# Optimization experiments

Hardware: AMD Instinct MI355X
Metric: run time of the kernel (lower is better)

Reference implementation:

```python
import jax, jax.numpy as jnp
import numpy as np

K = 3; PAD = 1; STRIDE = 1; EPS = 1e-5


def setup_inputs() -> dict:
    key = jax.random.key(0)
    k0, k1, k2 = jax.random.split(key, 3)
    B, C, H, W, O = 4, 256, 64, 64, 256
    x = jax.random.normal(k0, (B, C, H, W), jnp.float32)
    # offset conv: small random weights so offsets are nontrivial but bounded
    w_off = jax.random.normal(k1, (2 * K * K, C, K, K), jnp.float32) * 0.01
    b_off = jnp.zeros((2 * K * K,), jnp.float32)
    # kaiming normal, mode=fan_out: std = sqrt(2 / (O*K*K))
    w_def = jax.random.normal(k2, (O, C, K, K), jnp.float32) * np.float32(np.sqrt(2.0 / (O * K * K)))
    gamma = jnp.ones((O,), jnp.float32)
    beta = jnp.zeros((O,), jnp.float32)
    return {"x": x, "w_off": w_off, "b_off": b_off, "w_def": w_def, "gamma": gamma, "beta": beta}


def _bilinear_gather(x, py, px):
    """x: [B,C,H,W]; py,px: [B,K2,Ho,Wo] float sample coords.
    Returns [B,K2,Ho,Wo,C] with zero padding outside (per-corner masking,
    matching torchvision deform_conv2d)."""
    B, C, H, W = x.shape
    y0f = jnp.floor(py); x0f = jnp.floor(px)
    wy1 = py - y0f; wy0 = 1.0 - wy1
    wx1 = px - x0f; wx0 = 1.0 - wx1
    bidx = jnp.arange(B)[:, None, None, None]

    def corner(yf, xf, wgt):
        valid = (yf >= 0) & (yf <= H - 1) & (xf >= 0) & (xf <= W - 1)
        yc = jnp.clip(yf.astype(jnp.int32), 0, H - 1)
        xc = jnp.clip(xf.astype(jnp.int32), 0, W - 1)
        v = x[bidx, :, yc, xc]  # [B,K2,Ho,Wo,C] (advanced idx moves C last)
        return v * (wgt * valid)[..., None]

    return (corner(y0f, x0f, wy0 * wx0) + corner(y0f, x0f + 1.0, wy0 * wx1)
            + corner(y0f + 1.0, x0f, wy1 * wx0) + corner(y0f + 1.0, x0f + 1.0, wy1 * wx1))


def _forward(x, w_off, b_off, w_def, gamma, beta):
    B, C, H, W = x.shape
    O = w_def.shape[0]
    K2 = K * K
    # 1) offset-predicting conv
    off = jax.lax.conv_general_dilated(x, w_off, (STRIDE, STRIDE), ((PAD, PAD), (PAD, PAD)))
    off = off + b_off[None, :, None, None]
    Ho, Wo = off.shape[2], off.shape[3]
    off = off.reshape(B, K2, 2, Ho, Wo)  # pairs (dy, dx) per kernel tap
    # 2) deformable sampling locations
    ky, kx = jnp.meshgrid(jnp.arange(K, dtype=jnp.float32), jnp.arange(K, dtype=jnp.float32), indexing='ij')
    base_y = (jnp.arange(Ho, dtype=jnp.float32) * STRIDE - PAD)
    base_x = (jnp.arange(Wo, dtype=jnp.float32) * STRIDE - PAD)
    py = off[:, :, 0] + ky.reshape(K2)[None, :, None, None] + base_y[None, None, :, None]
    px = off[:, :, 1] + kx.reshape(K2)[None, :, None, None] + base_x[None, None, None, :]
    vals = _bilinear_gather(x, py, px)  # [B,K2,Ho,Wo,C]
    # 3) deform conv GEMM (bias=False)
    out = jnp.einsum('bkhwc,ock->bohw', vals, w_def.reshape(O, C, K2))
    # 4) BatchNorm (training mode: batch stats) + ReLU
    mean = out.mean(axis=(0, 2, 3))
    var = out.var(axis=(0, 2, 3))
    out = (out - mean[None, :, None, None]) * (gamma * jax.lax.rsqrt(var + EPS))[None, :, None, None]
    out = out + beta[None, :, None, None]
    return jax.nn.relu(out)


def reference(x, w_off, b_off, w_def, gamma, beta):
    return _forward(x, w_off, b_off, w_def, gamma, beta)
```

## Files before the change

kernel.cpp:

```cpp
#include <hip/hip_runtime.h>
#include <hip/hip_bf16.h>

typedef unsigned int  uint;
typedef unsigned short ushort;
typedef short bf16x8 __attribute__((ext_vector_type(8)));
typedef float f32x4  __attribute__((ext_vector_type(4)));

#define HW   4096
#define KD   2304

__device__ __forceinline__ void load_lds16(const void* g, void* l) {
    __builtin_amdgcn_global_load_lds((const __attribute__((address_space(1))) void*)g,
                                     (__attribute__((address_space(3))) void*)l, 16, 0, 0);
}
__device__ __forceinline__ float blo(uint u) { return __uint_as_float(u << 16); }
__device__ __forceinline__ float bhi(uint u) { return __uint_as_float(u & 0xffff0000u); }
__device__ __forceinline__ uint pack2(float e, float o) {
    __hip_bfloat16 he = __float2bfloat16(e), ho = __float2bfloat16(o);
    return (uint)(*(ushort*)&he) | ((uint)(*(ushort*)&ho) << 16);
}

__global__ __launch_bounds__(256) void prep_all(const float* __restrict__ x,
                                                const float* __restrict__ w_def,
                                                const float* __restrict__ w_off,
                                                uint* __restrict__ x2t,
                                                ushort* __restrict__ bt,
                                                ushort* __restrict__ bt0,
                                                float* __restrict__ stats) {
    __shared__ uint tl[32][65];
    int bid = blockIdx.x;
    int t = threadIdx.x;
    if (bid < 1024) {
        int ab  = bid & 63;
        int cpb = (bid >> 6) & 3;
        int b   = bid >> 8;
#pragma unroll
        for (int i = 0; i < 8; ++i) {
            int idx = i * 256 + t;
            int cp = idx >> 6, a = idx & 63;
            const float* p = x + ((size_t)(b * 256 + (cpb * 32 + cp) * 2)) * HW + ab * 64 + a;
            tl[cp][a] = pack2(p[0], p[HW]);
        }
        __syncthreads();
#pragma unroll
        for (int i = 0; i < 8; ++i) {
            int idx = i * 256 + t;
            int a = idx >> 5, cp = idx & 31;
            x2t[((size_t)b * 4096 + ab * 64 + a) * 128 + cpb * 32 + cp] = tl[cp][a];
        }
    } else if (bid < 3328) {
        int idx = (bid - 1024) * 256 + t;
        int c   = idx & 255;
        int tap = (idx >> 8) % 9;
        int o   = idx / KD;
        __hip_bfloat16 h = __float2bfloat16(w_def[(o * 256 + c) * 9 + tap]);
        bt[idx] = *(ushort*)&h;
    } else if (bid < 3616) {
        int idx = (bid - 3328) * 256 + t;
        int c   = idx & 255;
        int tap = (idx >> 8) % 9;
        int j   = idx / KD;
        float v = (j < 18) ? w_off[(j * 256 + c) * 9 + tap] : 0.f;
        __hip_bfloat16 h = __float2bfloat16(v);
        bt0[idx] = *(ushort*)&h;
    } else {
        float4 z = {0.f, 0.f, 0.f, 0.f};
        ((float4*)stats)[t] = z;
    }
}

__global__ __attribute__((amdgpu_waves_per_eu(4, 4))) __launch_bounds__(1024)
void fused_main(const uint* __restrict__ x2t,
                const ushort* __restrict__ bt,
                const ushort* __restrict__ bt0,
                const float* __restrict__ b_off,
                float* __restrict__ out,
                float* __restrict__ stats) {
    int id = blockIdx.x;
    int xcd = id & 7;
    int b = xcd >> 1, h = (xcd & 1) * 32 + (id >> 3);
    int t = threadIdx.x;
    int wv = t >> 6, lane = t & 63;
    int mrow = lane & 15, quad = lane >> 4;
    bool producer = (wv < 8);
    int ppos = (wv << 3) + (lane >> 3);
    int pc8  = lane & 7;
    int wvc  = wv - 8;

    __shared__ __align__(16) char smem[66048];
    uint*   lX   = (uint*)smem;
    ushort* lB0  = (ushort*)(smem + 24576);
    float*  sOff = (float*)(smem + 61440);
    int*    sAc  = (int*)smem;
    float*  sWc  = (float*)(smem + 9216);
    ushort* lA   = (ushort*)(smem + 18432);

    {
        f32x4 accO = {0.f, 0.f, 0.f, 0.f};
        int mq = wv & 3, nn = (wv >> 2) & 1;
        for (int cb = 0; cb < 4; ++cb) {
#pragma unroll
            for (int s = 0; s < 2; ++s) {
                int q = s * 16 + wv;
                if (q < 24) {
                    int dy  = q >> 3;
                    int y   = h + dy - 1;
                    int sub = q & 7;
                    int wl  = sub * 8 + (lane >> 3);
                    int cps = ((lane & 7) ^ ((lane >> 3) & 7)) * 4;
                    if ((unsigned)y < 64u) {
                        const uint* src = x2t + ((size_t)(b * 4096 + y * 64 + wl)) * 128 + cb * 32 + cps;
                        load_lds16(src, &lX[q * 256]);
                    } else {
                        uint4 z = {0u, 0u, 0u, 0u};
                        *(uint4*)&lX[q * 256 + lane * 4] = z;
                    }
                }
            }
#pragma unroll
            for (int s = 0; s < 3; ++s) {
                int q = s * 16 + wv;
                if (q < 36) {
                    int e = q * 512 + lane * 8;
                    int o  = e / 576;
                    int r  = e - o * 576;
                    int chp = r >> 3;
                    int ch  = chp ^ (o & 7);
                    int tap = ch >> 3, k8 = ch & 7;
                    const ushort* src = bt0 + (size_t)o * KD + tap * 256 + cb * 64 + k8 * 8;
                    load_lds16(src, &lB0[q * 512]);
                }
            }
            __syncthreads();
            if (producer) {
#pragma unroll
                for (int tap = 0; tap < 9; ++tap) {
                    int dy = tap / 3, dx = tap % 3;
                    int xx = mq * 16 + mrow + dx - 1;
                    bool vx = (unsigned)xx < 64u;
                    int xc = min(max(xx, 0), 63);
#pragma unroll
                    for (int kb = 0; kb < 2; ++kb) {
                        int cp0 = kb * 16 + quad * 4;
                        uint4 ad = {0u, 0u, 0u, 0u};
                        if (vx) ad = *(const uint4*)&lX[dy * 2048 + xc * 32 + (cp0 ^ ((xc & 7) * 4))];
                        bf16x8 af = *(bf16x8*)&ad;
                        int o = nn * 16 + mrow;
                        int chs = (tap * 8 + (((kb * 4 + quad)) ^ (o & 7)));
                        bf16x8 bfr = *(const bf16x8*)&lB0[o * 576 + chs * 8];
                        accO = __builtin_amdgcn_mfma_f32_16x16x32_bf16(af, bfr, accO, 0, 0, 0);
                    }
                }
            }
            __syncthreads();
        }
        if (producer) {
            int o = nn * 16 + mrow;
            if (o < 18) {
                float bias = b_off[o];
                int wpos = mq * 16 + quad * 4;
                sOff[o * 64 + wpos + 0] = accO.x + bias;
                sOff[o * 64 + wpos + 1] = accO.y + bias;
                sOff[o * 64 + wpos + 2] = accO.z + bias;
                sOff[o * 64 + wpos + 3] = accO.w + bias;
            }
        }
        __syncthreads();
    }

    for (int i = t; i < 576; i += 1024) {
        int tap = i >> 6, ww = i & 63;
        float oy = sOff[(2 * tap) * 64 + ww];
        float ox = sOff[(2 * tap + 1) * 64 + ww];
        float py = oy + (float)(tap / 3 + h - 1);
        float px = ox + (float)(tap % 3 + ww - 1);
        float y0f = floorf(py), x0f = floorf(px);
        float wy1 = py - y0f, wx1 = px - x0f;
        float wy0 = 1.f - wy1, wx0 = 1.f - wx1;
        bool vy0 = (y0f >= 0.f) && (y0f <= 63.f);
        bool vy1 = (y0f >= -1.f) && (y0f <= 62.f);
        bool vx0 = (x0f >= 0.f) && (x0f <= 63.f);
        bool vx1 = (x0f >= -1.f) && (x0f <= 62.f);
        int iy0 = min(max((int)y0f, 0), 63),  iy1 = min(max((int)y0f + 1, 0), 63);
        int ix0 = min(max((int)x0f, 0), 63),  ix1 = min(max((int)x0f + 1, 0), 63);
        sAc[0 * 576 + tap * 64 + ww] = iy0 * 64 + ix0;
        sAc[1 * 576 + tap * 64 + ww] = iy0 * 64 + ix1;
        sAc[2 * 576 + tap * 64 + ww] = iy1 * 64 + ix0;
        sAc[3 * 576 + tap * 64 + ww] = iy1 * 64 + ix1;
        sWc[0 * 576 + tap * 64 + ww] = wy0 * wx0 * (float)(vy0 && vx0);
        sWc[1 * 576 + tap * 64 + ww] = wy0 * wx1 * (float)(vy0 && vx1);
        sWc[2 * 576 + tap * 64 + ww] = wy1 * wx0 * (float)(vy1 && vx0);
        sWc[3 * 576 + tap * 64 + ww] = wy1 * wx1 * (float)(vy1 && vx1);
    }
    __syncthreads();

    f32x4 acc[4][2];
#pragma unroll
    for (int m = 0; m < 4; ++m)
#pragma unroll
        for (int n = 0; n < 2; ++n) acc[m][n] = {0.f, 0.f, 0.f, 0.f};

    const uint* xb = x2t + (size_t)b * 4096 * 128;

    auto issue_gathers = [&](int sl, uint4 (&g)[4]) {
        int tap = sl >> 2, cb = sl & 3;
        const uint* xp = xb + cb * 32 + pc8 * 4;
        g[0] = *(const uint4*)(xp + (size_t)sAc[0 * 576 + tap * 64 + ppos] * 128);
        g[1] = *(const uint4*)(xp + (size_t)sAc[1 * 576 + tap * 64 + ppos] * 128);
        g[2] = *(const uint4*)(xp + (size_t)sAc[2 * 576 + tap * 64 + ppos] * 128);
        g[3] = *(const uint4*)(xp + (size_t)sAc[3 * 576 + tap * 64 + ppos] * 128);
    };
    auto finish = [&](int sl, ushort* lAb, const uint4 (&g)[4]) {
        int tap = sl >> 2;
        float f0 = sWc[0 * 576 + tap * 64 + ppos], f1 = sWc[1 * 576 + tap * 64 + ppos];
        float f2 = sWc[2 * 576 + tap * 64 + ppos], f3 = sWc[3 * 576 + tap * 64 + ppos];
        const uint* c0 = (const uint*)&g[0];
        const uint* c1 = (const uint*)&g[1];
        const uint* c2 = (const uint*)&g[2];
        const uint* c3 = (const uint*)&g[3];
        uint r[4];
#pragma unroll
        for (int j = 0; j < 4; ++j) {
            float ev = f0 * blo(c0[j]) + f1 * blo(c1[j]) + f2 * blo(c2[j]) + f3 * blo(c3[j]);
            float ov = f0 * bhi(c0[j]) + f1 * bhi(c1[j]) + f2 * bhi(c2[j]) + f3 * bhi(c3[j]);
            r[j] = pack2(ev, ov);
        }
        uint4 gg = {r[0], r[1], r[2], r[3]};
        *(uint4*)&lAb[ppos * 64 + ((pc8 ^ (ppos & 7)) * 8)] = gg;
    };
    auto loadB = [&](int sl, bf16x8 (&br)[4]) {
        int tap = sl >> 2, cb = sl & 3;
        const ushort* base = bt + tap * 256 + cb * 64 + quad * 8;
#pragma unroll
        for (int kb = 0; kb < 2; ++kb)
#pragma unroll
            for (int n = 0; n < 2; ++n) {
                int r = wvc * 32 + n * 16 + mrow;
                br[kb * 2 + n] = *(const bf16x8*)(base + (size_t)r * KD + kb * 32);
            }
    };
    auto mfma_pass = [&](int bi, const bf16x8 (&br)[4]) {
#pragma unroll
        for (int kb = 0; kb < 2; ++kb) {
            bf16x8 af[4];
#pragma unroll
            for (int m = 0; m < 4; ++m) {
                int r = m * 16 + mrow;
                af[m] = *(const bf16x8*)&lA[bi * 4096 + r * 64 + (((kb * 4 + quad) ^ (r & 7)) * 8)];
            }
#pragma unroll
            for (int n = 0; n < 2; ++n)
#pragma unroll
                for (int m = 0; m < 4; ++m)
                    acc[m][n] = __builtin_amdgcn_mfma_f32_16x16x32_bf16(af[m], br[kb * 2 + n], acc[m][n], 0, 0, 0);
        }
    };

    uint4 gA[4];
    bf16x8 brA[4], brB[4];
    if (producer) {
        issue_gathers(0, gA);
        finish(0, &lA[0], gA);
        issue_gathers(1, gA);
        finish(1, &lA[4096], gA);
        asm volatile("s_waitcnt lgkmcnt(0)" ::: "memory");
    } else {
        loadB(0, brA);
        loadB(1, brB);
    }
    __builtin_amdgcn_s_barrier();
    __builtin_amdgcn_sched_barrier(0);

    for (int s = 0; s < 36; s += 2) {
        if (producer) {
            if (s + 2 < 36) {
                issue_gathers(s + 2, gA);
                finish(s + 2, &lA[((s + 2) & 3) * 4096], gA);
                issue_gathers(s + 3, gA);
                finish(s + 3, &lA[((s + 3) & 3) * 4096], gA);
                asm volatile("s_waitcnt lgkmcnt(0)" ::: "memory");
            }
        } else {
            __builtin_amdgcn_s_setprio(1);
            mfma_pass(s & 3, brA);
            mfma_pass((s + 1) & 3, brB);
            __builtin_amdgcn_s_setprio(0);
            if (s + 2 < 36) loadB(s + 2, brA);
            if (s + 3 < 36) loadB(s + 3, brB);
        }
        __builtin_amdgcn_s_barrier();
        __builtin_amdgcn_sched_barrier(0);
    }

    if (!producer) {
#pragma unroll
        for (int n = 0; n < 2; ++n) {
            int o = wvc * 32 + n * 16 + mrow;
            float ss = 0.f, qq = 0.f;
#pragma unroll
            for (int m = 0; m < 4; ++m) {
                int pos = m * 16 + quad * 4;
                f32x4 v = acc[m][n];
                *(f32x4*)(out + ((size_t)(b * 256 + o)) * HW + h * 64 + pos) = v;
                ss += v.x + v.y + v.z + v.w;
                qq += v.x * v.x + v.y * v.y + v.z * v.z + v.w * v.w;
            }
            ss += __shfl_xor(ss, 16); ss += __shfl_xor(ss, 32);
            qq += __shfl_xor(qq, 16); qq += __shfl_xor(qq, 32);
            if (quad == 0) {
                atomicAdd(&stats[o], ss);
                atomicAdd(&stats[512 + o], qq);
            }
        }
    }
}

__global__ __launch_bounds__(256) void bn_apply(float* __restrict__ out,
                                                const float* __restrict__ stats,
                                                const float* __restrict__ gamma,
                                                const float* __restrict__ beta) {
    int bid = blockIdx.x;
    int o = (bid >> 2) & 255;
    float S = stats[o], S2 = stats[512 + o];
    float mu  = S * (1.f / 16384.f);
    float var = S2 * (1.f / 16384.f) - mu * mu;
    float sc  = gamma[o] * rsqrtf(var + 1e-5f);
    float be  = beta[o];
    int idx4 = bid * 256 + threadIdx.x;
    float4 v = ((const float4*)out)[idx4];
    v.x = fmaxf((v.x - mu) * sc + be, 0.f);
    v.y = fmaxf((v.y - mu) * sc + be, 0.f);
    v.z = fmaxf((v.z - mu) * sc + be, 0.f);
    v.w = fmaxf((v.w - mu) * sc + be, 0.f);
    ((float4*)out)[idx4] = v;
}

extern "C" void kernel_launch(void* const* d_in, const int* in_sizes, int n_in,
                              void* d_out, int out_size, void* d_ws, size_t ws_size,
                              hipStream_t stream) {
    const float* x     = (const float*)d_in[0];
    const float* w_off = (const float*)d_in[1];
    const float* b_off = (const float*)d_in[2];
    const float* w_def = (const float*)d_in[3];
    const float* gamma = (const float*)d_in[4];
    const float* beta  = (const float*)d_in[5];
    float* out = (float*)d_out;

    char* ws = (char*)d_ws;
    uint*   x2t   = (uint*)ws;
    ushort* bt    = (ushort*)(ws + 8388608);
    ushort* bt0   = (ushort*)(ws + 9568256);
    float*  stats = (float*)(ws + 9715712);

    prep_all  <<<3617, 256, 0, stream>>>(x, w_def, w_off, x2t, bt, bt0, stats);
    fused_main<<<256, 1024, 0, stream>>>(x2t, bt, bt0, b_off, out, stats);
    bn_apply  <<<4096, 256, 0, stream>>>(out, stats, gamma, beta);
}
```

Measured before the change: 144.6 us.

## Split each row's output channels across two 512-thread blocks

```diff
diff --git a/kernel.cpp b/kernel.cpp
--- a/kernel.cpp
+++ b/kernel.cpp
@@ -69,7 +69,7 @@
     }
 }
 
-__global__ __attribute__((amdgpu_waves_per_eu(4, 4))) __launch_bounds__(1024)
+__global__ __attribute__((amdgpu_waves_per_eu(4, 4))) __launch_bounds__(512)
 void fused_main(const uint* __restrict__ x2t,
                 const ushort* __restrict__ bt,
                 const ushort* __restrict__ bt0,
@@ -77,15 +77,16 @@
                 float* __restrict__ out,
                 float* __restrict__ stats) {
     int id = blockIdx.x;
-    int xcd = id & 7;
-    int b = xcd >> 1, h = (xcd & 1) * 32 + (id >> 3);
+    int nh = id & 1;
+    int bid2 = id >> 1;
+    int xcd = bid2 & 7;
+    int b = xcd >> 1, h = (xcd & 1) * 32 + (bid2 >> 3);
     int t = threadIdx.x;
     int wv = t >> 6, lane = t & 63;
     int mrow = lane & 15, quad = lane >> 4;
-    bool producer = (wv < 8);
-    int ppos = (wv << 3) + (lane >> 3);
+    bool producer = (wv < 4);
     int pc8  = lane & 7;
-    int wvc  = wv - 8;
+    int wvc  = wv - 4;
 
     __shared__ __align__(16) char smem[66048];
     uint*   lX   = (uint*)smem;
@@ -97,29 +98,27 @@
 
     {
         f32x4 accO = {0.f, 0.f, 0.f, 0.f};
-        int mq = wv & 3, nn = (wv >> 2) & 1;
+        int mq = wv & 3, nn = wv >> 2;
         for (int cb = 0; cb < 4; ++cb) {
 #pragma unroll
-            for (int s = 0; s < 2; ++s) {
-                int q = s * 16 + wv;
-                if (q < 24) {
-                    int dy  = q >> 3;
-                    int y   = h + dy - 1;
-                    int sub = q & 7;
-                    int wl  = sub * 8 + (lane >> 3);
-                    int cps = ((lane & 7) ^ ((lane >> 3) & 7)) * 4;
-                    if ((unsigned)y < 64u) {
-                        const uint* src = x2t + ((size_t)(b * 4096 + y * 64 + wl)) * 128 + cb * 32 + cps;
-                        load_lds16(src, &lX[q * 256]);
-                    } else {
-                        uint4 z = {0u, 0u, 0u, 0u};
-                        *(uint4*)&lX[q * 256 + lane * 4] = z;
-                    }
+            for (int s = 0; s < 3; ++s) {
+                int q   = s * 8 + wv;
+                int dy  = q >> 3;
+                int y   = h + dy - 1;
+                int sub = q & 7;
+                int wl  = sub * 8 + (lane >> 3);
+                int cps = ((lane & 7) ^ ((lane >> 3) & 7)) * 4;
+                if ((unsigned)y < 64u) {
+                    const uint* src = x2t + ((size_t)(b * 4096 + y * 64 + wl)) * 128 + cb * 32 + cps;
+                    load_lds16(src, &lX[q * 256]);
+                } else {
+                    uint4 z = {0u, 0u, 0u, 0u};
+                    *(uint4*)&lX[q * 256 + lane * 4] = z;
                 }
             }
 #pragma unroll
-            for (int s = 0; s < 3; ++s) {
-                int q = s * 16 + wv;
+            for (int s = 0; s < 5; ++s) {
+                int q = s * 8 + wv;
                 if (q < 36) {
                     int e = q * 512 + lane * 8;
                     int o  = e / 576;
@@ -132,33 +131,31 @@
                 }
             }
             __syncthreads();
-            if (producer) {
-#pragma unroll
-                for (int tap = 0; tap < 9; ++tap) {
-                    int dy = tap / 3, dx = tap % 3;
-                    int xx = mq * 16 + mrow + dx - 1;
-                    bool vx = (unsigned)xx < 64u;
-                    int xc = min(max(xx, 0), 63);
-#pragma unroll
-                    for (int kb = 0; kb < 2; ++kb) {
-                        int cp0 = kb * 16 + quad * 4;
-                        uint4 ad = {0u, 0u, 0u, 0u};
-                        if (vx) ad = *(const uint4*)&lX[dy * 2048 + xc * 32 + (cp0 ^ ((xc & 7) * 4))];
-                        bf16x8 af = *(bf16x8*)&ad;
-                        int o = nn * 16 + mrow;
-                        int chs = (tap * 8 + (((kb * 4 + quad)) ^ (o & 7)));
-                        bf16x8 bfr = *(const bf16x8*)&lB0[o * 576 + chs * 8];
-                        accO = __builtin_amdgcn_mfma_f32_16x16x32_bf16(af, bfr, accO, 0, 0, 0);
-                    }
+#pragma unroll
+            for (int tap = 0; tap < 9; ++tap) {
+                int dy = tap / 3, dx = tap % 3;
+                int xx = mq * 16 + mrow + dx - 1;
+                bool vx = (unsigned)xx < 64u;
+                int xc = min(max(xx, 0), 63);
+#pragma unroll
+                for (int kb = 0; kb < 2; ++kb) {
+                    int cp0 = kb * 16 + quad * 4;
+                    uint4 ad = {0u, 0u, 0u, 0u};
+                    if (vx) ad = *(const uint4*)&lX[dy * 2048 + xc * 32 + (cp0 ^ ((xc & 7) * 4))];
+                    bf16x8 af = *(bf16x8*)&ad;
+                    int o = nn * 16 + mrow;
+                    int chs = (tap * 8 + (((kb * 4 + quad)) ^ (o & 7)));
+                    bf16x8 bfr = *(const bf16x8*)&lB0[o * 576 + chs * 8];
+                    accO = __builtin_amdgcn_mfma_f32_16x16x32_bf16(af, bfr, accO, 0, 0, 0);
                 }
             }
             __syncthreads();
         }
-        if (producer) {
-            int o = nn * 16 + mrow;
+        {
+            int o = (wv >> 2) * 16 + mrow;
             if (o < 18) {
                 float bias = b_off[o];
-                int wpos = mq * 16 + quad * 4;
+                int wpos = (wv & 3) * 16 + quad * 4;
                 sOff[o * 64 + wpos + 0] = accO.x + bias;
                 sOff[o * 64 + wpos + 1] = accO.y + bias;
                 sOff[o * 64 + wpos + 2] = accO.z + bias;
@@ -168,7 +165,7 @@
         __syncthreads();
     }
 
-    for (int i = t; i < 576; i += 1024) {
+    for (int i = t; i < 576; i += 512) {
         int tap = i >> 6, ww = i & 63;
         float oy = sOff[(2 * tap) * 64 + ww];
         float ox = sOff[(2 * tap + 1) * 64 + ww];
@@ -202,16 +199,18 @@
 
     const uint* xb = x2t + (size_t)b * 4096 * 128;
 
-    auto issue_gathers = [&](int sl, uint4 (&g)[4]) {
+    auto issue_gathers = [&](int sl, int h2, uint4 (&g)[4]) {
         int tap = sl >> 2, cb = sl & 3;
+        int ppos = (wv << 4) + (h2 << 3) + (lane >> 3);
         const uint* xp = xb + cb * 32 + pc8 * 4;
         g[0] = *(const uint4*)(xp + (size_t)sAc[0 * 576 + tap * 64 + ppos] * 128);
         g[1] = *(const uint4*)(xp + (size_t)sAc[1 * 576 + tap * 64 + ppos] * 128);
         g[2] = *(const uint4*)(xp + (size_t)sAc[2 * 576 + tap * 64 + ppos] * 128);
         g[3] = *(const uint4*)(xp + (size_t)sAc[3 * 576 + tap * 64 + ppos] * 128);
     };
-    auto finish = [&](int sl, ushort* lAb, const uint4 (&g)[4]) {
+    auto finish = [&](int sl, int h2, ushort* lAb, const uint4 (&g)[4]) {
         int tap = sl >> 2;
+        int ppos = (wv << 4) + (h2 << 3) + (lane >> 3);
         float f0 = sWc[0 * 576 + tap * 64 + ppos], f1 = sWc[1 * 576 + tap * 64 + ppos];
         float f2 = sWc[2 * 576 + tap * 64 + ppos], f3 = sWc[3 * 576 + tap * 64 + ppos];
         const uint* c0 = (const uint*)&g[0];
@@ -228,9 +227,16 @@
         uint4 gg = {r[0], r[1], r[2], r[3]};
         *(uint4*)&lAb[ppos * 64 + ((pc8 ^ (ppos & 7)) * 8)] = gg;
     };
+    auto stage_slice = [&](int sl, ushort* lAb) {
+        uint4 g0[4], g1[4];
+        issue_gathers(sl, 0, g0);
+        issue_gathers(sl, 1, g1);
+        finish(sl, 0, lAb, g0);
+        finish(sl, 1, lAb, g1);
+    };
     auto loadB = [&](int sl, bf16x8 (&br)[4]) {
         int tap = sl >> 2, cb = sl & 3;
-        const ushort* base = bt + tap * 256 + cb * 64 + quad * 8;
+        const ushort* base = bt + (size_t)(nh * 128) * KD + tap * 256 + cb * 64 + quad * 8;
 #pragma unroll
         for (int kb = 0; kb < 2; ++kb)
 #pragma unroll
@@ -256,13 +262,10 @@
         }
     };
 
-    uint4 gA[4];
     bf16x8 brA[4], brB[4];
     if (producer) {
-        issue_gathers(0, gA);
-        finish(0, &lA[0], gA);
-        issue_gathers(1, gA);
-        finish(1, &lA[4096], gA);
+        stage_slice(0, &lA[0]);
+        stage_slice(1, &lA[4096]);
         asm volatile("s_waitcnt lgkmcnt(0)" ::: "memory");
     } else {
         loadB(0, brA);
@@ -274,10 +277,8 @@
     for (int s = 0; s < 36; s += 2) {
         if (producer) {
             if (s + 2 < 36) {
-                issue_gathers(s + 2, gA);
-                finish(s + 2, &lA[((s + 2) & 3) * 4096], gA);
-                issue_gathers(s + 3, gA);
-                finish(s + 3, &lA[((s + 3) & 3) * 4096], gA);
+                stage_slice(s + 2, &lA[((s + 2) & 3) * 4096]);
+                stage_slice(s + 3, &lA[((s + 3) & 3) * 4096]);
                 asm volatile("s_waitcnt lgkmcnt(0)" ::: "memory");
             }
         } else {
@@ -295,7 +296,7 @@
     if (!producer) {
 #pragma unroll
         for (int n = 0; n < 2; ++n) {
-            int o = wvc * 32 + n * 16 + mrow;
+            int o = nh * 128 + wvc * 32 + n * 16 + mrow;
             float ss = 0.f, qq = 0.f;
 #pragma unroll
             for (int m = 0; m < 4; ++m) {
@@ -353,6 +354,6 @@
     float*  stats = (float*)(ws + 9715712);
 
     prep_all  <<<3617, 256, 0, stream>>>(x, w_def, w_off, x2t, bt, bt0, stats);
-    fused_main<<<256, 1024, 0, stream>>>(x2t, bt, bt0, b_off, out, stats);
+    fused_main<<<512, 512, 0, stream>>>(x2t, bt, bt0, b_off, out, stats);
     bn_apply  <<<4096, 256, 0, stream>>>(out, stats, gamma, beta);
 }
```

Measured after the change: 167.8 us. 1.16x slower.
